# Kernel tuning notes

Measured on AMD Instinct MI355X. Metric: run time of the kernel, lower is better.

The kernel has to match this reference:

```python
import jax, jax.numpy as jnp
import numpy as np

B, DIN, DM, N, L, H = 4, 256, 256, 256, 64, 4
LH = L // H  # d_k per head = 16


def setup_inputs() -> dict:
    key = jax.random.key(0)
    ks = jax.random.split(key, 11)
    randn = lambda k, s: jax.random.normal(k, s, dtype=jnp.float32)
    return {
        "X_Query": randn(ks[0], (B, DIN, N, L)),
        "X_Key": randn(ks[1], (B, DIN, N, L)),
        "X_Value": randn(ks[2], (B, DIN, N, L)),
        "Wq": randn(ks[3], (DM, DIN)) * 0.05,
        "bq": randn(ks[4], (DM,)) * 0.05,
        "Wk": randn(ks[5], (DM, DIN)) * 0.05,
        "bk": randn(ks[6], (DM,)) * 0.05,
        "Wv": randn(ks[7], (DM, DIN)) * 0.05,
        "bv": randn(ks[8], (DM,)) * 0.05,
        "Wo": randn(ks[9], (DM, DM)) * 0.05,
        "bo": randn(ks[10], (DM,)) * 0.05,
    }


def _conv1x1(x, W, b):
    # x: (B, Cin, N, L); 1x1 Conv2d == per-position linear over channels
    return jnp.einsum("bcnl,oc->bonl", x, W) + b[None, :, None, None]


def reference(X_Query, X_Key, X_Value, Wq, bq, Wk, bk, Wv, bv, Wo, bo):
    q = _conv1x1(X_Query, Wq, bq)  # (B, DM, N, L)
    k = _conv1x1(X_Key, Wk, bk)
    v = _conv1x1(X_Value, Wv, bv)
    # torch: chunk(num_heads, dim=-1) then cat(dim=0) -> head axis from L split
    split = lambda x: x.reshape(B, DM, N, H, LH)
    qh, kh, vh = split(q), split(k), split(v)
    # attention over the CHANNEL axis (d_model x d_model scores per point/head)
    scale = 1.0 / np.sqrt(LH).astype(np.float32)
    scores = jnp.einsum("bdnhl,benhl->bnhde", qh, kh) * scale  # (B,N,H,DM,DM)
    p = jax.nn.softmax(scores, axis=-1)
    o = jnp.einsum("bnhde,benhl->bdnhl", p, vh)  # (B,DM,N,H,LH)
    attention_heads = o.reshape(B, DM, N, L)  # cat heads back along L
    return _conv1x1(attention_heads, Wo, bo)
```

## Files before the change

### kernel.cpp

```cpp
#include <hip/hip_runtime.h>


typedef unsigned int u32;
typedef unsigned short u16;
typedef __attribute__((ext_vector_type(8))) short s8v;
typedef __attribute__((ext_vector_type(16))) float f16v;

#define XS 0
#define QT 8192
#define KT 16384
#define VT 24576
#define LDS_TOT 33792
#define LSTR 36

__device__ __forceinline__ u16 f2bf(float x) {
  union { float f; u32 u; } c; c.f = x;
  return (u16)((c.u + 0x7FFFu + ((c.u >> 16) & 1u)) >> 16);
}
__device__ __forceinline__ u32 pk2(float a, float b) {
  return (u32)f2bf(a) | ((u32)f2bf(b) << 16);
}

__global__ void cvt_weights(const float* __restrict__ wq, const float* __restrict__ wk,
                            const float* __restrict__ wv, const float* __restrict__ wo,
                            u16* __restrict__ out) {
  int i = blockIdx.x * 256 + threadIdx.x;
  out[i]          = f2bf(wq[i]);
  out[i + 65536]  = f2bf(wk[i]);
  out[i + 131072] = f2bf(wv[i]);
  out[i + 196608] = f2bf(wo[i]);
}

__device__ __forceinline__ void stage_lin(const float* __restrict__ src, u16* lds,
                                          int linoff, int tid) {
#pragma unroll
  for (int it = 0; it < 4; ++it) {
    int f4 = it * 512 + tid;
    int c = f4 >> 3;
    int l4 = (f4 & 7) << 2;
    const float4 v = *reinterpret_cast<const float4*>(src + c * 16384 + l4);
    uint2 w; w.x = pk2(v.x, v.y); w.y = pk2(v.z, v.w);
    *reinterpret_cast<uint2*>(&lds[linoff + c * LSTR + l4]) = w;
  }
}

__device__ __forceinline__ void lin_to_xs(u16* lds, int linoff, int tid) {
#pragma unroll
  for (int it = 0; it < 2; ++it) {
    int idx = it * 512 + tid;
    int l = idx & 31, cb = idx >> 5;
    int sb = linoff + cb * (8 * LSTR) + l;
    u32 u0 = (u32)lds[sb]            | ((u32)lds[sb + LSTR]     << 16);
    u32 u1 = (u32)lds[sb + 2 * LSTR] | ((u32)lds[sb + 3 * LSTR] << 16);
    u32 u2 = (u32)lds[sb + 4 * LSTR] | ((u32)lds[sb + 5 * LSTR] << 16);
    u32 u3 = (u32)lds[sb + 6 * LSTR] | ((u32)lds[sb + 7 * LSTR] << 16);
    union { u32 u[4]; s8v v; } pw;
    pw.u[0] = u0; pw.u[1] = u1; pw.u[2] = u2; pw.u[3] = u3;
    *reinterpret_cast<s8v*>(&lds[XS + cb * 256 + l * 8]) = pw.v;
  }
}

__device__ __forceinline__ void proj_T(u16* lds, const u16* __restrict__ w,
                                       const float* __restrict__ bias, int dst,
                                       int wid, int lo, int hi) {
  const int o = wid * 32 + lo;
  f16v a;
#pragma unroll
  for (int i = 0; i < 16; ++i) a[i] = 0.f;
#pragma unroll
  for (int s = 0; s < 16; ++s) {
    const s8v bw = *reinterpret_cast<const s8v*>(w + o * 256 + s * 16 + hi * 8);
    const s8v xf = *reinterpret_cast<const s8v*>(&lds[XS + (2 * s + hi) * 256 + lo * 8]);
    a = __builtin_amdgcn_mfma_f32_32x32x16_bf16(xf, bw, a, 0, 0, 0);
  }
  const float bb = bias[o];
#pragma unroll
  for (int g = 0; g < 4; ++g) {
    uint2 wv2;
    wv2.x = pk2(a[4 * g + 0] + bb, a[4 * g + 1] + bb);
    wv2.y = pk2(a[4 * g + 2] + bb, a[4 * g + 3] + bb);
    *reinterpret_cast<uint2*>(&lds[dst + g * 2048 + o * 8 + hi * 4]) = wv2;
  }
}

__device__ __forceinline__ void proj_V(u16* lds, const u16* __restrict__ w,
                                       const float* __restrict__ bias,
                                       int wid, int lo, int hi) {
  const int e0 = wid * 32;
  const int e = e0 + lo;
  f16v a;
#pragma unroll
  for (int i = 0; i < 16; ++i) a[i] = 0.f;
#pragma unroll
  for (int s = 0; s < 16; ++s) {
    const s8v aw = *reinterpret_cast<const s8v*>(w + e * 256 + s * 16 + hi * 8);
    const s8v xf = *reinterpret_cast<const s8v*>(&lds[XS + (2 * s + hi) * 256 + lo * 8]);
    a = __builtin_amdgcn_mfma_f32_32x32x16_bf16(aw, xf, a, 0, 0, 0);
  }
#pragma unroll
  for (int g = 0; g < 4; ++g) {
    const int eb = e0 + 8 * g + 4 * hi;
    uint2 wv2;
    wv2.x = pk2(a[4 * g + 0] + bias[eb + 0], a[4 * g + 1] + bias[eb + 1]);
    wv2.y = pk2(a[4 * g + 2] + bias[eb + 2], a[4 * g + 3] + bias[eb + 3]);
    *reinterpret_cast<uint2*>(&lds[VT + (4 * wid + g) * 256 + lo * 8 + hi * 4]) = wv2;
  }
}

__device__ __forceinline__ void proj_O(u16* lds, const u16* __restrict__ w,
                                       const float* __restrict__ bias,
                                       float* __restrict__ out, long obase,
                                       int wid, int lo, int hi) {
  const int o0 = wid * 32;
  const int o = o0 + lo;
  f16v a;
#pragma unroll
  for (int i = 0; i < 16; ++i) a[i] = 0.f;
#pragma unroll
  for (int s = 0; s < 16; ++s) {
    const s8v aw = *reinterpret_cast<const s8v*>(w + o * 256 + s * 16 + hi * 8);
    const s8v bf = *reinterpret_cast<const s8v*>(&lds[XS + (2 * s + hi) * 256 + lo * 8]);
    a = __builtin_amdgcn_mfma_f32_32x32x16_bf16(aw, bf, a, 0, 0, 0);
  }
#pragma unroll
  for (int r = 0; r < 16; ++r) {
    const int orow = o0 + (r & 3) + 8 * (r >> 2) + 4 * hi;
    out[obase + orow * 16384 + lo] = a[r] + bias[orow];
  }
}

__global__ __launch_bounds__(512)
void mha_kernel(const float* __restrict__ xq, const float* __restrict__ xk,
                const float* __restrict__ xv, const u16* __restrict__ wb,
                const float* __restrict__ bq, const float* __restrict__ bk,
                const float* __restrict__ bv, const float* __restrict__ bo,
                float* __restrict__ out) {
  __shared__ __align__(16) u16 lds[LDS_TOT];
  const int tid = threadIdx.x;
  const int lane = tid & 63;
  const int wid = tid >> 6;
  const int lo = lane & 31;
  const int hi = lane >> 5;
  const int hp = blockIdx.x & 1;
  const int n = (blockIdx.x >> 1) & 255;
  const int b = blockIdx.x >> 9;
  const long base = (long)b * 4194304 + n * 64 + hp * 32;

  stage_lin(xq + base, lds, KT, tid);
  __syncthreads();
  lin_to_xs(lds, KT, tid);
  __syncthreads();
  stage_lin(xk + base, lds, KT, tid);
  proj_T(lds, wb + 0, bq, QT, wid, lo, hi);
  __syncthreads();
  lin_to_xs(lds, KT, tid);
  __syncthreads();
  stage_lin(xv + base, lds, VT, tid);
  proj_T(lds, wb + 65536, bk, KT, wid, lo, hi);
  __syncthreads();
  lin_to_xs(lds, VT, tid);
  __syncthreads();
  proj_V(lds, wb + 131072, bv, wid, lo, hi);
  __syncthreads();

  f16v z16;
#pragma unroll
  for (int i = 0; i < 16; ++i) z16[i] = 0.f;
  const int l15 = lane & 15;

#pragma unroll
  for (int h = 0; h < 2; ++h) {
    const s8v qf = *reinterpret_cast<const s8v*>(
        &lds[QT + (2 * h + hi) * 2048 + (wid * 32 + lo) * 8]);
    float m = -3.0e38f, sum = 0.f;
    f16v ot;
#pragma unroll
    for (int i = 0; i < 16; ++i) ot[i] = 0.f;

#pragma unroll
    for (int et = 0; et < 8; ++et) {
      const s8v kf = *reinterpret_cast<const s8v*>(
          &lds[KT + (2 * h + hi) * 2048 + (et * 32 + lo) * 8]);
      f16v st = __builtin_amdgcn_mfma_f32_32x32x16_bf16(kf, qf, z16, 0, 0, 0);

      float tmax = st[0];
#pragma unroll
      for (int i = 1; i < 16; ++i) tmax = fmaxf(tmax, st[i]);
      tmax = fmaxf(tmax, __shfl_xor(tmax, 32));
      const float mn = fmaxf(m, tmax);
      const float f = __expf(0.25f * (m - mn));
      m = mn;
      sum *= f;
#pragma unroll
      for (int i = 0; i < 16; ++i) ot[i] *= f;
      float ts = 0.f;
#pragma unroll
      for (int i = 0; i < 16; ++i) {
        const float p = __expf(0.25f * (st[i] - m));
        st[i] = p;
        ts += p;
      }
      sum += ts;

#pragma unroll
      for (int s2 = 0; s2 < 2; ++s2) {
        const int s = 2 * et + s2;
        const s8v vf = *reinterpret_cast<const s8v*>(
            &lds[VT + (2 * s + hi) * 256 + (h * 16 + l15) * 8]);
        const int q = s2 * 8;
        const u32 x0 = pk2(st[q + 0], st[q + 1]);
        const u32 x1 = pk2(st[q + 2], st[q + 3]);
        const u32 y0 = pk2(st[q + 4], st[q + 5]);
        const u32 y1 = pk2(st[q + 6], st[q + 7]);
        const u32 sx0 = (u32)__shfl_xor((int)x0, 32);
        const u32 sx1 = (u32)__shfl_xor((int)x1, 32);
        const u32 sy0 = (u32)__shfl_xor((int)y0, 32);
        const u32 sy1 = (u32)__shfl_xor((int)y1, 32);
        union { u32 u[4]; s8v v; } bu;
        bu.u[0] = hi ? sy0 : x0;
        bu.u[1] = hi ? sy1 : x1;
        bu.u[2] = hi ? y0 : sx0;
        bu.u[3] = hi ? y1 : sx1;
        ot = __builtin_amdgcn_mfma_f32_32x32x16_bf16(vf, bu.v, ot, 0, 0, 0);
      }
    }
    sum += __shfl_xor(sum, 32);
    const float rinv = 1.0f / sum;
#pragma unroll
    for (int r = 0; r < 8; ++r) {
      const int lh = (r & 3) + 8 * (r >> 2) + 4 * hi;
      const int l = h * 16 + lh;
      const int d = wid * 32 + lo;
      lds[XS + (d >> 3) * 256 + l * 8 + (d & 7)] = f2bf(ot[r] * rinv);
    }
  }
  __syncthreads();

  proj_O(lds, wb + 196608, bo, out, base, wid, lo, hi);
}

extern "C" void kernel_launch(void* const* d_in, const int* in_sizes, int n_in,
                              void* d_out, int out_size, void* d_ws, size_t ws_size,
                              hipStream_t stream) {
  const float* xq = (const float*)d_in[0];
  const float* xk = (const float*)d_in[1];
  const float* xv = (const float*)d_in[2];
  const float* wq = (const float*)d_in[3];
  const float* bq = (const float*)d_in[4];
  const float* wk = (const float*)d_in[5];
  const float* bk = (const float*)d_in[6];
  const float* wv = (const float*)d_in[7];
  const float* bv = (const float*)d_in[8];
  const float* wo = (const float*)d_in[9];
  const float* bo = (const float*)d_in[10];
  u16* wsb = (u16*)d_ws;
  float* out = (float*)d_out;

  cvt_weights<<<dim3(256), dim3(256), 0, stream>>>(wq, wk, wv, wo, wsb);
  mha_kernel<<<dim3(2048), dim3(512), 0, stream>>>(xq, xk, xv, wsb, bq, bk, bv, bo, out);
}
```

Measured before the change: 213.0 us.

## Fold softmax scale into Q, use exp2, interleave both heads in attention loop

Q is scaled by 0.25*log2(e) at projection time so the softmax can use a raw exp2 with no per-element multiply. The two head loops are merged into one key-tile loop, so the two heads' independent MFMA and softmax chains can overlap. Max and sum reductions become trees, and the first tile skips the rescale. This adds live registers (two accumulators and two score tiles), which may lower occupancy. Q also takes an extra bf16 rounding after scaling.

After: 357.8 us. 1.68x slower.

```diff
diff --git a/kernel.cpp b/kernel.cpp
--- a/kernel.cpp
+++ b/kernel.cpp
@@ -13,12 +13,21 @@
 #define LDS_TOT 33792
 #define LSTR 36
 
+#define QSCALE 0.360673760222f
+
 __device__ __forceinline__ u16 f2bf(float x) {
   union { float f; u32 u; } c; c.f = x;
   return (u16)((c.u + 0x7FFFu + ((c.u >> 16) & 1u)) >> 16);
 }
 __device__ __forceinline__ u32 pk2(float a, float b) {
   return (u32)f2bf(a) | ((u32)f2bf(b) << 16);
+}
+
+__device__ __forceinline__ float xh_max(float v) {
+  return fmaxf(v, __shfl_xor(v, 32));
+}
+__device__ __forceinline__ float xh_sum(float v) {
+  return v + __shfl_xor(v, 32);
 }
 
 __global__ void cvt_weights(const float* __restrict__ wq, const float* __restrict__ wk,
@@ -62,7 +71,7 @@
 
 __device__ __forceinline__ void proj_T(u16* lds, const u16* __restrict__ w,
                                        const float* __restrict__ bias, int dst,
-                                       int wid, int lo, int hi) {
+                                       float osc, int wid, int lo, int hi) {
   const int o = wid * 32 + lo;
   f16v a;
 #pragma unroll
@@ -77,8 +86,8 @@
 #pragma unroll
   for (int g = 0; g < 4; ++g) {
     uint2 wv2;
-    wv2.x = pk2(a[4 * g + 0] + bb, a[4 * g + 1] + bb);
-    wv2.y = pk2(a[4 * g + 2] + bb, a[4 * g + 3] + bb);
+    wv2.x = pk2((a[4 * g + 0] + bb) * osc, (a[4 * g + 1] + bb) * osc);
+    wv2.y = pk2((a[4 * g + 2] + bb) * osc, (a[4 * g + 3] + bb) * osc);
     *reinterpret_cast<uint2*>(&lds[dst + g * 2048 + o * 8 + hi * 4]) = wv2;
   }
 }
@@ -151,12 +160,12 @@
   lin_to_xs(lds, KT, tid);
   __syncthreads();
   stage_lin(xk + base, lds, KT, tid);
-  proj_T(lds, wb + 0, bq, QT, wid, lo, hi);
+  proj_T(lds, wb + 0, bq, QT, QSCALE, wid, lo, hi);
   __syncthreads();
   lin_to_xs(lds, KT, tid);
   __syncthreads();
   stage_lin(xv + base, lds, VT, tid);
-  proj_T(lds, wb + 65536, bk, KT, wid, lo, hi);
+  proj_T(lds, wb + 65536, bk, KT, 1.0f, wid, lo, hi);
   __syncthreads();
   lin_to_xs(lds, VT, tid);
   __syncthreads();
@@ -168,50 +177,67 @@
   for (int i = 0; i < 16; ++i) z16[i] = 0.f;
   const int l15 = lane & 15;
 
+  s8v qf[2];
+  qf[0] = *reinterpret_cast<const s8v*>(&lds[QT + (0 + hi) * 2048 + (wid * 32 + lo) * 8]);
+  qf[1] = *reinterpret_cast<const s8v*>(&lds[QT + (2 + hi) * 2048 + (wid * 32 + lo) * 8]);
+
+  f16v ot[2];
+  float m[2], sm[2];
 #pragma unroll
   for (int h = 0; h < 2; ++h) {
-    const s8v qf = *reinterpret_cast<const s8v*>(
-        &lds[QT + (2 * h + hi) * 2048 + (wid * 32 + lo) * 8]);
-    float m = -3.0e38f, sum = 0.f;
-    f16v ot;
-#pragma unroll
-    for (int i = 0; i < 16; ++i) ot[i] = 0.f;
-
-#pragma unroll
-    for (int et = 0; et < 8; ++et) {
+#pragma unroll
+    for (int i = 0; i < 16; ++i) ot[h][i] = 0.f;
+    m[h] = 0.f; sm[h] = 0.f;
+  }
+
+#pragma unroll
+  for (int et = 0; et < 8; ++et) {
+    f16v st[2];
+#pragma unroll
+    for (int h = 0; h < 2; ++h) {
       const s8v kf = *reinterpret_cast<const s8v*>(
           &lds[KT + (2 * h + hi) * 2048 + (et * 32 + lo) * 8]);
-      f16v st = __builtin_amdgcn_mfma_f32_32x32x16_bf16(kf, qf, z16, 0, 0, 0);
-
-      float tmax = st[0];
-#pragma unroll
-      for (int i = 1; i < 16; ++i) tmax = fmaxf(tmax, st[i]);
-      tmax = fmaxf(tmax, __shfl_xor(tmax, 32));
-      const float mn = fmaxf(m, tmax);
-      const float f = __expf(0.25f * (m - mn));
-      m = mn;
-      sum *= f;
-#pragma unroll
-      for (int i = 0; i < 16; ++i) ot[i] *= f;
-      float ts = 0.f;
-#pragma unroll
-      for (int i = 0; i < 16; ++i) {
-        const float p = __expf(0.25f * (st[i] - m));
-        st[i] = p;
-        ts += p;
+      st[h] = __builtin_amdgcn_mfma_f32_32x32x16_bf16(kf, qf[h], z16, 0, 0, 0);
+    }
+#pragma unroll
+    for (int h = 0; h < 2; ++h) {
+      float t[8];
+#pragma unroll
+      for (int i = 0; i < 8; ++i) t[i] = fmaxf(st[h][i], st[h][i + 8]);
+#pragma unroll
+      for (int i = 0; i < 4; ++i) t[i] = fmaxf(t[i], t[i + 4]);
+      float tm = xh_max(fmaxf(fmaxf(t[0], t[1]), fmaxf(t[2], t[3])));
+
+      if (et == 0) {
+        m[h] = tm;
+      } else {
+        const float mn = fmaxf(m[h], tm);
+        const float f = __builtin_amdgcn_exp2f(m[h] - mn);
+        m[h] = mn;
+        sm[h] *= f;
+#pragma unroll
+        for (int i = 0; i < 16; ++i) ot[h][i] *= f;
       }
-      sum += ts;
+      float p[16];
+#pragma unroll
+      for (int i = 0; i < 16; ++i) p[i] = __builtin_amdgcn_exp2f(st[h][i] - m[h]);
+      float s[8];
+#pragma unroll
+      for (int i = 0; i < 8; ++i) s[i] = p[i] + p[i + 8];
+#pragma unroll
+      for (int i = 0; i < 4; ++i) s[i] = s[i] + s[i + 4];
+      sm[h] += (s[0] + s[1]) + (s[2] + s[3]);
 
 #pragma unroll
       for (int s2 = 0; s2 < 2; ++s2) {
-        const int s = 2 * et + s2;
+        const int ks = 2 * et + s2;
         const s8v vf = *reinterpret_cast<const s8v*>(
-            &lds[VT + (2 * s + hi) * 256 + (h * 16 + l15) * 8]);
+            &lds[VT + (2 * ks + hi) * 256 + (h * 16 + l15) * 8]);
         const int q = s2 * 8;
-        const u32 x0 = pk2(st[q + 0], st[q + 1]);
-        const u32 x1 = pk2(st[q + 2], st[q + 3]);
-        const u32 y0 = pk2(st[q + 4], st[q + 5]);
-        const u32 y1 = pk2(st[q + 6], st[q + 7]);
+        const u32 x0 = pk2(p[q + 0], p[q + 1]);
+        const u32 x1 = pk2(p[q + 2], p[q + 3]);
+        const u32 y0 = pk2(p[q + 4], p[q + 5]);
+        const u32 y1 = pk2(p[q + 6], p[q + 7]);
         const u32 sx0 = (u32)__shfl_xor((int)x0, 32);
         const u32 sx1 = (u32)__shfl_xor((int)x1, 32);
         const u32 sy0 = (u32)__shfl_xor((int)y0, 32);
@@ -221,17 +247,20 @@
         bu.u[1] = hi ? sy1 : x1;
         bu.u[2] = hi ? y0 : sx0;
         bu.u[3] = hi ? y1 : sx1;
-        ot = __builtin_amdgcn_mfma_f32_32x32x16_bf16(vf, bu.v, ot, 0, 0, 0);
+        ot[h] = __builtin_amdgcn_mfma_f32_32x32x16_bf16(vf, bu.v, ot[h], 0, 0, 0);
       }
     }
-    sum += __shfl_xor(sum, 32);
-    const float rinv = 1.0f / sum;
+  }
+
+#pragma unroll
+  for (int h = 0; h < 2; ++h) {
+    const float rinv = 1.0f / xh_sum(sm[h]);
+    const int d = wid * 32 + lo;
 #pragma unroll
     for (int r = 0; r < 8; ++r) {
       const int lh = (r & 3) + 8 * (r >> 2) + 4 * hi;
       const int l = h * 16 + lh;
-      const int d = wid * 32 + lo;
-      lds[XS + (d >> 3) * 256 + l * 8 + (d & 7)] = f2bf(ot[r] * rinv);
+      lds[XS + (d >> 3) * 256 + l * 8 + (d & 7)] = f2bf(ot[h][r] * rinv);
     }
   }
   __syncthreads();
```

## Keep Q fragments in registers, fold scale into Q, use exp2 softmax

Applied to the files above, without the earlier changes.

Q projection results are rearranged via cross-half-wave shuffles directly into MFMA operand fragments held in registers, removing the Q tile from LDS and shrinking shared memory from about 33.8K to 25.6K u16 elements. The softmax scale and log2(e) are folded into Q so the inner loop uses raw exp2 without per-element multiplies, and the first tile skips the rescale. Shuffle count per P-pack is halved, max/sum reductions use tree form, and launch bounds request 6 waves per SIMD to allow more resident blocks. Risks: extra registers for the Q fragments and possible spills under the tighter launch bound.

After: 390.8 us. +83.4%, slower.

```diff
diff --git a/kernel.cpp b/kernel.cpp
--- a/kernel.cpp
+++ b/kernel.cpp
@@ -7,11 +7,14 @@
 typedef __attribute__((ext_vector_type(16))) float f16v;
 
 #define XS 0
-#define QT 8192
-#define KT 16384
-#define VT 24576
-#define LDS_TOT 33792
+#define KT 8192
+#define VT 16384
+#define LINQ 8192
+#define LINKV 16384
+#define LDS_TOT 25600
 #define LSTR 36
+
+#define QSCALE 0.360673760222f
 
 __device__ __forceinline__ u16 f2bf(float x) {
   union { float f; u32 u; } c; c.f = x;
@@ -20,6 +23,8 @@
 __device__ __forceinline__ u32 pk2(float a, float b) {
   return (u32)f2bf(a) | ((u32)f2bf(b) << 16);
 }
+__device__ __forceinline__ float xh_max(float v) { return fmaxf(v, __shfl_xor(v, 32)); }
+__device__ __forceinline__ float xh_sum(float v) { return v + __shfl_xor(v, 32); }
 
 __global__ void cvt_weights(const float* __restrict__ wq, const float* __restrict__ wk,
                             const float* __restrict__ wv, const float* __restrict__ wo,
@@ -60,9 +65,9 @@
   }
 }
 
-__device__ __forceinline__ void proj_T(u16* lds, const u16* __restrict__ w,
-                                       const float* __restrict__ bias, int dst,
-                                       int wid, int lo, int hi) {
+__device__ __forceinline__ void proj_Q(u16* lds, const u16* __restrict__ w,
+                                       const float* __restrict__ bias,
+                                       s8v qf[2], int wid, int lo, int hi) {
   const int o = wid * 32 + lo;
   f16v a;
 #pragma unroll
@@ -74,12 +79,48 @@
     a = __builtin_amdgcn_mfma_f32_32x32x16_bf16(xf, bw, a, 0, 0, 0);
   }
   const float bb = bias[o];
+  u32 W[8];
+#pragma unroll
+  for (int g = 0; g < 4; ++g) {
+    W[2 * g]     = pk2((a[4 * g + 0] + bb) * QSCALE, (a[4 * g + 1] + bb) * QSCALE);
+    W[2 * g + 1] = pk2((a[4 * g + 2] + bb) * QSCALE, (a[4 * g + 3] + bb) * QSCALE);
+  }
+#pragma unroll
+  for (int h = 0; h < 2; ++h) {
+    const int bse = 4 * h;
+    const u32 z0 = hi ? W[bse + 0] : W[bse + 2];
+    const u32 z1 = hi ? W[bse + 1] : W[bse + 3];
+    const u32 s0 = (u32)__shfl_xor((int)z0, 32);
+    const u32 s1 = (u32)__shfl_xor((int)z1, 32);
+    union { u32 u[4]; s8v v; } fu;
+    fu.u[0] = hi ? s0 : W[bse + 0];
+    fu.u[1] = hi ? s1 : W[bse + 1];
+    fu.u[2] = hi ? W[bse + 2] : s0;
+    fu.u[3] = hi ? W[bse + 3] : s1;
+    qf[h] = fu.v;
+  }
+}
+
+__device__ __forceinline__ void proj_K(u16* lds, const u16* __restrict__ w,
+                                       const float* __restrict__ bias,
+                                       int wid, int lo, int hi) {
+  const int o = wid * 32 + lo;
+  f16v a;
+#pragma unroll
+  for (int i = 0; i < 16; ++i) a[i] = 0.f;
+#pragma unroll
+  for (int s = 0; s < 16; ++s) {
+    const s8v bw = *reinterpret_cast<const s8v*>(w + o * 256 + s * 16 + hi * 8);
+    const s8v xf = *reinterpret_cast<const s8v*>(&lds[XS + (2 * s + hi) * 256 + lo * 8]);
+    a = __builtin_amdgcn_mfma_f32_32x32x16_bf16(xf, bw, a, 0, 0, 0);
+  }
+  const float bb = bias[o];
 #pragma unroll
   for (int g = 0; g < 4; ++g) {
     uint2 wv2;
     wv2.x = pk2(a[4 * g + 0] + bb, a[4 * g + 1] + bb);
     wv2.y = pk2(a[4 * g + 2] + bb, a[4 * g + 3] + bb);
-    *reinterpret_cast<uint2*>(&lds[dst + g * 2048 + o * 8 + hi * 4]) = wv2;
+    *reinterpret_cast<uint2*>(&lds[KT + g * 2048 + o * 8 + hi * 4]) = wv2;
   }
 }
 
@@ -129,7 +170,7 @@
   }
 }
 
-__global__ __launch_bounds__(512)
+__global__ __launch_bounds__(512, 6)
 void mha_kernel(const float* __restrict__ xq, const float* __restrict__ xk,
                 const float* __restrict__ xv, const u16* __restrict__ wb,
                 const float* __restrict__ bq, const float* __restrict__ bk,
@@ -146,19 +187,20 @@
   const int b = blockIdx.x >> 9;
   const long base = (long)b * 4194304 + n * 64 + hp * 32;
 
-  stage_lin(xq + base, lds, KT, tid);
-  __syncthreads();
-  lin_to_xs(lds, KT, tid);
-  __syncthreads();
-  stage_lin(xk + base, lds, KT, tid);
-  proj_T(lds, wb + 0, bq, QT, wid, lo, hi);
-  __syncthreads();
-  lin_to_xs(lds, KT, tid);
-  __syncthreads();
-  stage_lin(xv + base, lds, VT, tid);
-  proj_T(lds, wb + 65536, bk, KT, wid, lo, hi);
-  __syncthreads();
-  lin_to_xs(lds, VT, tid);
+  stage_lin(xq + base, lds, LINQ, tid);
+  __syncthreads();
+  lin_to_xs(lds, LINQ, tid);
+  __syncthreads();
+  s8v qf[2];
+  stage_lin(xk + base, lds, LINKV, tid);
+  proj_Q(lds, wb + 0, bq, qf, wid, lo, hi);
+  __syncthreads();
+  lin_to_xs(lds, LINKV, tid);
+  __syncthreads();
+  stage_lin(xv + base, lds, LINKV, tid);
+  proj_K(lds, wb + 65536, bk, wid, lo, hi);
+  __syncthreads();
+  lin_to_xs(lds, LINKV, tid);
   __syncthreads();
   proj_V(lds, wb + 131072, bv, wid, lo, hi);
   __syncthreads();
@@ -170,9 +212,7 @@
 
 #pragma unroll
   for (int h = 0; h < 2; ++h) {
-    const s8v qf = *reinterpret_cast<const s8v*>(
-        &lds[QT + (2 * h + hi) * 2048 + (wid * 32 + lo) * 8]);
-    float m = -3.0e38f, sum = 0.f;
+    float m = 0.f, sm = 0.f;
     f16v ot;
 #pragma unroll
     for (int i = 0; i < 16; ++i) ot[i] = 0.f;
@@ -181,56 +221,62 @@
     for (int et = 0; et < 8; ++et) {
       const s8v kf = *reinterpret_cast<const s8v*>(
           &lds[KT + (2 * h + hi) * 2048 + (et * 32 + lo) * 8]);
-      f16v st = __builtin_amdgcn_mfma_f32_32x32x16_bf16(kf, qf, z16, 0, 0, 0);
-
-      float tmax = st[0];
-#pragma unroll
-      for (int i = 1; i < 16; ++i) tmax = fmaxf(tmax, st[i]);
-      tmax = fmaxf(tmax, __shfl_xor(tmax, 32));
-      const float mn = fmaxf(m, tmax);
-      const float f = __expf(0.25f * (m - mn));
-      m = mn;
-      sum *= f;
-#pragma unroll
-      for (int i = 0; i < 16; ++i) ot[i] *= f;
-      float ts = 0.f;
-#pragma unroll
-      for (int i = 0; i < 16; ++i) {
-        const float p = __expf(0.25f * (st[i] - m));
-        st[i] = p;
-        ts += p;
+      f16v st = __builtin_amdgcn_mfma_f32_32x32x16_bf16(kf, qf[h], z16, 0, 0, 0);
+
+      float t[8];
+#pragma unroll
+      for (int i = 0; i < 8; ++i) t[i] = fmaxf(st[i], st[i + 8]);
+#pragma unroll
+      for (int i = 0; i < 4; ++i) t[i] = fmaxf(t[i], t[i + 4]);
+      const float tm = xh_max(fmaxf(fmaxf(t[0], t[1]), fmaxf(t[2], t[3])));
+
+      if (et == 0) {
+        m = tm;
+      } else {
+        const float mn = fmaxf(m, tm);
+        const float f = __builtin_amdgcn_exp2f(m - mn);
+        m = mn;
+        sm *= f;
+#pragma unroll
+        for (int i = 0; i < 16; ++i) ot[i] *= f;
       }
-      sum += ts;
+#pragma unroll
+      for (int i = 0; i < 16; ++i) st[i] = __builtin_amdgcn_exp2f(st[i] - m);
+      float s[8];
+#pragma unroll
+      for (int i = 0; i < 8; ++i) s[i] = st[i] + st[i + 8];
+#pragma unroll
+      for (int i = 0; i < 4; ++i) s[i] = s[i] + s[i + 4];
+      sm += (s[0] + s[1]) + (s[2] + s[3]);
 
 #pragma unroll
       for (int s2 = 0; s2 < 2; ++s2) {
-        const int s = 2 * et + s2;
+        const int ks = 2 * et + s2;
         const s8v vf = *reinterpret_cast<const s8v*>(
-            &lds[VT + (2 * s + hi) * 256 + (h * 16 + l15) * 8]);
+            &lds[VT + (2 * ks + hi) * 256 + (h * 16 + l15) * 8]);
         const int q = s2 * 8;
         const u32 x0 = pk2(st[q + 0], st[q + 1]);
         const u32 x1 = pk2(st[q + 2], st[q + 3]);
         const u32 y0 = pk2(st[q + 4], st[q + 5]);
         const u32 y1 = pk2(st[q + 6], st[q + 7]);
-        const u32 sx0 = (u32)__shfl_xor((int)x0, 32);
-        const u32 sx1 = (u32)__shfl_xor((int)x1, 32);
-        const u32 sy0 = (u32)__shfl_xor((int)y0, 32);
-        const u32 sy1 = (u32)__shfl_xor((int)y1, 32);
+        const u32 z0 = hi ? x0 : y0;
+        const u32 z1 = hi ? x1 : y1;
+        const u32 s0 = (u32)__shfl_xor((int)z0, 32);
+        const u32 s1 = (u32)__shfl_xor((int)z1, 32);
         union { u32 u[4]; s8v v; } bu;
-        bu.u[0] = hi ? sy0 : x0;
-        bu.u[1] = hi ? sy1 : x1;
-        bu.u[2] = hi ? y0 : sx0;
-        bu.u[3] = hi ? y1 : sx1;
+        bu.u[0] = hi ? s0 : x0;
+        bu.u[1] = hi ? s1 : x1;
+        bu.u[2] = hi ? y0 : s0;
+        bu.u[3] = hi ? y1 : s1;
         ot = __builtin_amdgcn_mfma_f32_32x32x16_bf16(vf, bu.v, ot, 0, 0, 0);
       }
     }
-    sum += __shfl_xor(sum, 32);
-    const float rinv = 1.0f / sum;
+    const float rinv = 1.0f / xh_sum(sm);
+    const int d = wid * 32 + lo;
 #pragma unroll
     for (int r = 0; r < 8; ++r) {
       const int lh = (r & 3) + 8 * (r >> 2) + 4 * hi;
       const int l = h * 16 + lh;
-      const int d = wid * 32 + lo;
       lds[XS + (d >> 3) * 256 + l * 8 + (d & 7)] = f2bf(ot[r] * rinv);
     }
   }
```
